# Kernel tuning notes

Hardware: AMD Instinct MI355X
Metric: run time of the kernel (lower is better)

## Reference

```python
import jax, jax.numpy as jnp
import numpy as np

B, N, D_IN, H, R = 4096, 32, 256, 256, 3
VIRTUAL_DECAY = 0.7


def setup_inputs() -> dict:
    key = jax.random.key(0)
    ks = jax.random.split(key, 16)
    def xavier(k, shape):
        fan_in, fan_out = shape[-1], shape[-2]
        lim = np.sqrt(6.0 / (fan_in + fan_out))
        return jax.random.uniform(k, shape, jnp.float32, -lim, lim)
    return {
        'input_vec': jax.random.normal(ks[0], (B, D_IN), jnp.float32),
        'child_h': jax.random.normal(ks[1], (B, N, H), jnp.float32),
        'child_c': jax.random.normal(ks[2], (B, N, H), jnp.float32),
        'relation_ids': jax.random.randint(ks[3], (B, N), 0, R, jnp.int32),
        'virtual_mask': jax.random.randint(ks[4], (B, N), 0, 2, jnp.int32).astype(bool),
        'rel_emb': xavier(ks[5], (R, H)),
        'W_i': xavier(ks[6], (H, D_IN + H)), 'b_i': jnp.full((H,), 0.1, jnp.float32),
        'W_f': xavier(ks[7], (R, H, H)),     'b_f': jnp.full((R, H), 0.1, jnp.float32),
        'W_o': xavier(ks[8], (H, D_IN + H)), 'b_o': jnp.full((H,), 0.1, jnp.float32),
        'W_u': xavier(ks[9], (H, D_IN + H)), 'b_u': jnp.full((H,), 0.1, jnp.float32),
        'w_att': xavier(ks[10], (1, H)).reshape(H), 'b_att': jnp.full((1,), 0.1, jnp.float32),
    }


def reference(input_vec, child_h, child_c, relation_ids, virtual_mask,
              rel_emb, W_i, b_i, W_f, b_f, W_o, b_o, W_u, b_u, w_att, b_att):
    # virtual-node decay applied to both child states
    decay = jnp.where(virtual_mask, VIRTUAL_DECAY, 1.0)[..., None]          # (B,N,1)
    ch = child_h * decay                                                     # (B,N,H)
    cc = child_c * decay                                                     # (B,N,H)

    # relation-aware attention over children (softmax over child axis)
    re = rel_emb[relation_ids]                                               # (B,N,H)
    scores = jnp.einsum('bnh,h->bn', re + ch, w_att) + b_att[0]              # (B,N)
    attn = jax.nn.softmax(scores, axis=1)[..., None]                         # (B,N,1)
    child_h_sum = jnp.sum(ch * attn, axis=1)                                 # (B,H)

    # relation-routed forget gates: compute all R linears, gather by relation id
    # NOTE: original applies NO sigmoid to f (faithful to source)
    f_all = jnp.einsum('bnh,rgh->bnrg', ch, W_f) + b_f                       # (B,N,R,H)
    f = jnp.take_along_axis(f_all, relation_ids[:, :, None, None], axis=2)[:, :, 0, :]  # (B,N,H)
    child_c_sum = jnp.sum(f * cc, axis=1)                                    # (B,H)

    combined = jnp.concatenate([input_vec, child_h_sum], axis=-1)            # (B,D_IN+H)
    i = jax.nn.sigmoid(combined @ W_i.T + b_i)
    o = jax.nn.sigmoid(combined @ W_o.T + b_o)
    u = jnp.tanh(combined @ W_u.T + b_u)
    c = i * u + child_c_sum
    h = o * jnp.tanh(c)
    return (h, c)
```

## Files before the change

kernel.cpp:

```cpp
#include <hip/hip_runtime.h>
#include <hip/hip_bf16.h>
#include <math.h>


#define B_    4096
#define N_    32
#define H_    256
#define DIN_  256
#define R_    3
#define MB    16
#define NBC   2
#define CHUNKS (MB / NBC)
#define DECAY 0.7f

#define WS_WF   0
#define WS_WI   196608
#define WS_WO   327680
#define WS_WU   458752
#define WS_ELEMS 589824

typedef __bf16 bf16;
typedef bf16  bf16x8 __attribute__((ext_vector_type(8)));
typedef float f32x4  __attribute__((ext_vector_type(4)));

__device__ __forceinline__ float sigmoidf_(float x) { return 1.0f / (1.0f + __expf(-x)); }

__device__ __forceinline__ bf16x8 cvt8_nt(const float* p) {
    f32x4 a = __builtin_nontemporal_load((const f32x4*)p);
    f32x4 b = __builtin_nontemporal_load((const f32x4*)(p + 4));
    bf16x8 r;
    #pragma unroll
    for (int j = 0; j < 4; ++j) { r[j] = (bf16)a[j]; r[j + 4] = (bf16)b[j]; }
    return r;
}
__device__ __forceinline__ bf16x8 cvt8_c(const float* p) {
    f32x4 a = *(const f32x4*)p;
    f32x4 b = *(const f32x4*)(p + 4);
    bf16x8 r;
    #pragma unroll
    for (int j = 0; j < 4; ++j) { r[j] = (bf16)a[j]; r[j + 4] = (bf16)b[j]; }
    return r;
}

template<bool WSW>
__device__ __forceinline__ bf16x8 ldw8(const bf16* wsp, const float* fp, int idx) {
    if constexpr (WSW) return *(const bf16x8*)(wsp + idx);
    else               return cvt8_c(fp + idx);
}

__global__ __launch_bounds__(256) void wprep(
    const float* __restrict__ Wf, const float* __restrict__ Wi,
    const float* __restrict__ Wo, const float* __restrict__ Wu,
    bf16* __restrict__ ws)
{
    int i = (blockIdx.x * 256 + threadIdx.x) * 8;
    const float* src; int off;
    if      (i < WS_WI) { src = Wf; off = i - WS_WF; }
    else if (i < WS_WO) { src = Wi; off = i - WS_WI; }
    else if (i < WS_WU) { src = Wo; off = i - WS_WO; }
    else                { src = Wu; off = i - WS_WU; }
    *(bf16x8*)(ws + i) = cvt8_c(src + off);
}

template<bool WSW>
__global__ __launch_bounds__(512, 4) void fused_main(
    const float* __restrict__ ivec,
    const float* __restrict__ child_h, const float* __restrict__ child_c,
    const int*  __restrict__ rel_ids,  const void* __restrict__ vmaskp,
    const float* __restrict__ rel_emb,
    const float* __restrict__ W_i, const float* __restrict__ b_i,
    const float* __restrict__ W_f, const float* __restrict__ b_f,
    const float* __restrict__ W_o, const float* __restrict__ b_o,
    const float* __restrict__ W_u, const float* __restrict__ b_u,
    const float* __restrict__ w_att, const float* __restrict__ b_att,
    const bf16* __restrict__ ws, float* __restrict__ out)
{
    __shared__ __align__(16) bf16 chs[NBC][N_][264];
    __shared__ __align__(16) bf16 hsumL[MB][264];
    __shared__ float csL[MB][H_];
    __shared__ float watt[H_];
    __shared__ float bfl[R_][H_];
    __shared__ float dall[MB][N_];
    __shared__ int   rids[MB][N_];
    __shared__ float scoreT[NBC][N_];
    __shared__ float attnd[NBC][N_];
    __shared__ float rdotL[4];
    __shared__ int   m8flag;

    const int tid  = threadIdx.x;
    const int wave = tid >> 6;
    const int lane = tid & 63;
    const int t    = lane & 15;
    const int q    = lane >> 4;
    const int b0   = blockIdx.x * MB;

    const bf16* wfb = ws + WS_WF;
    const bf16* wib = ws + WS_WI;
    const bf16* wob = ws + WS_WO;
    const bf16* wub = ws + WS_WU;

    if (tid < 64) {
        const unsigned char* vb = (const unsigned char*)vmaskp;
        int bad = vb[tid * 4 + 1] | vb[tid * 4 + 2] | vb[tid * 4 + 3];
        unsigned long long any = __ballot(bad != 0);
        if (tid == 0) m8flag = (any != 0ull) ? 1 : 0;
    }
    __syncthreads();

    if (tid < H_) watt[tid] = w_att[tid];
    {
        int idx = b0 * N_ + tid;
        rids[tid >> 5][tid & 31] = rel_ids[idx];
        bool vm = m8flag ? (((const unsigned char*)vmaskp)[idx] != 0)
                         : (((const int*)vmaskp)[idx] != 0);
        dall[tid >> 5][tid & 31] = vm ? DECAY : 1.0f;
    }
    if (tid >= 512 - R_ * 64 && false) {}
    for (int i = tid; i < R_ * H_; i += 512) ((float*)bfl)[i] = b_f[i];
    if (tid == 0) rdotL[3] = b_att[0];
    __syncthreads();

    if (wave < R_) {
        int r = wave;
        float p = 0.f;
        #pragma unroll
        for (int j = 0; j < 4; ++j) {
            int h = lane * 4 + j;
            p += rel_emb[r * H_ + h] * watt[h];
        }
        #pragma unroll
        for (int off = 32; off >= 1; off >>= 1) p += __shfl_xor(p, off);
        if (lane == 0) rdotL[r] = p;
    }

    for (int ck = 0; ck < CHUNKS; ++ck) {
        __syncthreads();

        {
            size_t base = (size_t)(b0 + ck * NBC) * (N_ * H_);
            #pragma unroll
            for (int it = 0; it < 4; ++it) {
                int ge = (it * 512 + tid) << 3;
                int bi = ge >> 13, n = (ge >> 8) & 31, h = ge & 255;
                *(bf16x8*)(&chs[bi][n][h]) = cvt8_nt(child_h + base + ge);
            }
        }
        __syncthreads();

        {
            int pair = tid >> 3, part = tid & 7;
            int bi = pair >> 5, n = pair & 31;
            const bf16* row = chs[bi][n];
            float p = 0.f;
            #pragma unroll
            for (int jj = 0; jj < 4; ++jj) {
                bf16x8 v = *(const bf16x8*)(&row[part * 32 + jj * 8]);
                #pragma unroll
                for (int j = 0; j < 8; ++j) p += (float)v[j] * watt[part * 32 + jj * 8 + j];
            }
            p += __shfl_xor(p, 1);
            p += __shfl_xor(p, 2);
            p += __shfl_xor(p, 4);
            if (part == 0) scoreT[bi][n] = p;
        }
        __syncthreads();

        if (tid < NBC * N_) {
            int bi = tid >> 5, n = tid & 31;
            int bl = ck * NBC + bi;
            float d = dall[bl][n];
            float s = d * scoreT[bi][n] + rdotL[rids[bl][n]] + rdotL[3];
            float m = s;
            #pragma unroll
            for (int off = 16; off >= 1; off >>= 1) m = fmaxf(m, __shfl_xor(m, off));
            float e = __expf(s - m);
            float sum = e;
            #pragma unroll
            for (int off = 16; off >= 1; off >>= 1) sum += __shfl_xor(sum, off);
            attnd[bi][n] = (e / sum) * d;
        }
        __syncthreads();

        {
            int bi = tid >> 8, g = tid & 255;
            int bl = ck * NBC + bi;
            float s = 0.f;
            #pragma unroll 8
            for (int n = 0; n < N_; ++n) s += attnd[bi][n] * (float)chs[bi][n][g];
            hsumL[bl][g] = (bf16)s;
        }

        f32x4 acc[2][4];
        #pragma unroll
        for (int i = 0; i < 2; ++i)
            #pragma unroll
            for (int j = 0; j < 4; ++j)
                #pragma unroll
                for (int c = 0; c < 4; ++c) acc[i][j][c] = 0.0f;

        bf16x8 bzero;
        #pragma unroll
        for (int i = 0; i < 8; ++i) bzero[i] = (bf16)0.0f;

        int myrid[4];
        #pragma unroll
        for (int nt = 0; nt < 4; ++nt)
            myrid[nt] = rids[ck * NBC + (nt >> 1)][((nt & 1) << 4) + t];

        #pragma unroll
        for (int kc = 0; kc < 8; ++kc) {
            const int k = kc * 32 + q * 8;
            bf16x8 v[4];
            #pragma unroll
            for (int nt = 0; nt < 4; ++nt)
                v[nt] = *(const bf16x8*)(&chs[nt >> 1][((nt & 1) << 4) + t][k]);
            #pragma unroll
            for (int r = 0; r < R_; ++r) {
                bf16x8 afrag[2];
                #pragma unroll
                for (int m2 = 0; m2 < 2; ++m2) {
                    int g = (wave * 2 + m2) * 16 + t;
                    afrag[m2] = ldw8<WSW>(wfb, W_f, (r * H_ + g) * H_ + k);
                }
                #pragma unroll
                for (int nt = 0; nt < 4; ++nt) {
                    bf16x8 vm = (myrid[nt] == r) ? v[nt] : bzero;
                    acc[0][nt] = __builtin_amdgcn_mfma_f32_16x16x32_bf16(afrag[0], vm, acc[0][nt], 0, 0, 0);
                    acc[1][nt] = __builtin_amdgcn_mfma_f32_16x16x32_bf16(afrag[1], vm, acc[1][nt], 0, 0, 0);
                }
            }
        }
        __syncthreads();

        {
            size_t base = (size_t)(b0 + ck * NBC) * (N_ * H_);
            #pragma unroll
            for (int it = 0; it < 4; ++it) {
                int ge = (it * 512 + tid) << 3;
                int bi = ge >> 13, n = (ge >> 8) & 31, h = ge & 255;
                *(bf16x8*)(&chs[bi][n][h]) = cvt8_nt(child_c + base + ge);
            }
        }
        __syncthreads();

        #pragma unroll
        for (int m2 = 0; m2 < 2; ++m2) {
            #pragma unroll
            for (int reg = 0; reg < 4; ++reg) {
                const int g = (wave * 2 + m2) * 16 + q * 4 + reg;
                #pragma unroll
                for (int bi = 0; bi < NBC; ++bi) {
                    int bl = ck * NBC + bi;
                    float p = 0.f;
                    #pragma unroll
                    for (int j = 0; j < 2; ++j) {
                        int nt = bi * 2 + j;
                        int n  = (j << 4) + t;
                        float Q   = acc[m2][nt][reg];
                        float d   = dall[bl][n];
                        float ccv = (float)chs[bi][n][g];
                        float bfv = bfl[rids[bl][n]][g];
                        p += ccv * d * fmaf(d, Q, bfv);
                    }
                    p += __shfl_xor(p, 1);
                    p += __shfl_xor(p, 2);
                    p += __shfl_xor(p, 4);
                    p += __shfl_xor(p, 8);
                    if (t == 0) csL[bl][g] = p;
                }
            }
        }
    }
    __syncthreads();

    const int j0 = wave * 32;
    f32x4 accI[2], accO[2], accU[2];
    #pragma unroll
    for (int c = 0; c < 2; ++c)
        #pragma unroll
        for (int r = 0; r < 4; ++r) { accI[c][r] = 0.f; accO[c][r] = 0.f; accU[c][r] = 0.f; }

    #pragma unroll
    for (int kc = 0; kc < 16; ++kc) {
        const int k = kc * 32 + q * 8;
        bf16x8 a;
        if (kc < 8) a = cvt8_nt(ivec + (size_t)(b0 + t) * DIN_ + k);
        else        a = *(const bf16x8*)(&hsumL[t][k - 256]);
        #pragma unroll
        for (int c = 0; c < 2; ++c) {
            int j = j0 + c * 16 + t;
            bf16x8 bI = ldw8<WSW>(wib, W_i, j * 512 + k);
            bf16x8 bO = ldw8<WSW>(wob, W_o, j * 512 + k);
            bf16x8 bU = ldw8<WSW>(wub, W_u, j * 512 + k);
            accI[c] = __builtin_amdgcn_mfma_f32_16x16x32_bf16(a, bI, accI[c], 0, 0, 0);
            accO[c] = __builtin_amdgcn_mfma_f32_16x16x32_bf16(a, bO, accO[c], 0, 0, 0);
            accU[c] = __builtin_amdgcn_mfma_f32_16x16x32_bf16(a, bU, accU[c], 0, 0, 0);
        }
    }

    #pragma unroll
    for (int c = 0; c < 2; ++c) {
        const int j = j0 + c * 16 + t;
        float biv = b_i[j], bov = b_o[j], buv = b_u[j];
        #pragma unroll
        for (int reg = 0; reg < 4; ++reg) {
            int bl = q * 4 + reg;
            size_t o1 = (size_t)(b0 + bl) * H_ + j;
            size_t o2 = (size_t)B_ * H_ + o1;
            float iv = sigmoidf_(accI[c][reg] + biv);
            float ov = sigmoidf_(accO[c][reg] + bov);
            float uv = tanhf(accU[c][reg] + buv);
            float cv = fmaf(iv, uv, csL[bl][j]);
            float hv = ov * tanhf(cv);
            __builtin_nontemporal_store(hv, out + o1);
            __builtin_nontemporal_store(cv, out + o2);
        }
    }
}

extern "C" void kernel_launch(void* const* d_in, const int* in_sizes, int n_in,
                              void* d_out, int out_size, void* d_ws, size_t ws_size,
                              hipStream_t stream)
{
    const float* ivec    = (const float*)d_in[0];
    const float* child_h = (const float*)d_in[1];
    const float* child_c = (const float*)d_in[2];
    const int*   relids  = (const int*)d_in[3];
    const void*  vmask   = d_in[4];
    const float* rel_emb = (const float*)d_in[5];
    const float* W_i     = (const float*)d_in[6];
    const float* b_i     = (const float*)d_in[7];
    const float* W_f     = (const float*)d_in[8];
    const float* b_f     = (const float*)d_in[9];
    const float* W_o     = (const float*)d_in[10];
    const float* b_o     = (const float*)d_in[11];
    const float* W_u     = (const float*)d_in[12];
    const float* b_u     = (const float*)d_in[13];
    const float* w_att   = (const float*)d_in[14];
    const float* b_att   = (const float*)d_in[15];
    float* out = (float*)d_out;
    bf16*  ws  = (bf16*)d_ws;

    const bool wsw = (ws_size >= (size_t)WS_ELEMS * sizeof(bf16));

    if (wsw) {
        hipLaunchKernelGGL(wprep, dim3(WS_ELEMS / 8 / 256), dim3(256), 0, stream,
                           W_f, W_i, W_o, W_u, ws);
        hipLaunchKernelGGL((fused_main<true>), dim3(B_ / MB), dim3(512), 0, stream,
                           ivec, child_h, child_c, relids, vmask, rel_emb,
                           W_i, b_i, W_f, b_f, W_o, b_o, W_u, b_u, w_att, b_att,
                           ws, out);
    } else {
        hipLaunchKernelGGL((fused_main<false>), dim3(B_ / MB), dim3(512), 0, stream,
                           ivec, child_h, child_c, relids, vmask, rel_emb,
                           W_i, b_i, W_f, b_f, W_o, b_o, W_u, b_u, w_att, b_att,
                           ws, out);
    }
}
```

Measured before the change: 484.7 us.

## Halve batch per block and prefetch child states into registers

Each block now handles 8 batch rows instead of 16, which doubles the grid and gives the GPU more blocks to keep it busy. The child_h and child_c loads are issued into registers early: child_c is fetched before the score and forget-gate MFMA work, and the next chunk's child_h is fetched during the reduction, so global memory latency overlaps with compute. The final gate GEMM still uses 16-row MFMA tiles, so half of its rows now duplicate real rows and only q<2 lanes store output. This wastes MFMA work and loads the weights once per 8 rows instead of per 16, which doubles total weight traffic. It also raises register pressure from the prefetch buffers.

```diff
diff --git a/kernel.cpp b/kernel.cpp
--- a/kernel.cpp
+++ b/kernel.cpp
@@ -8,7 +8,7 @@
 #define H_    256
 #define DIN_  256
 #define R_    3
-#define MB    16
+#define MB    8
 #define NBC   2
 #define CHUNKS (MB / NBC)
 #define DECAY 0.7f
@@ -107,15 +107,14 @@
     }
     __syncthreads();
 
-    if (tid < H_) watt[tid] = w_att[tid];
-    {
+    if (tid < 256) {
+        watt[tid] = w_att[tid];
         int idx = b0 * N_ + tid;
         rids[tid >> 5][tid & 31] = rel_ids[idx];
         bool vm = m8flag ? (((const unsigned char*)vmaskp)[idx] != 0)
                          : (((const int*)vmaskp)[idx] != 0);
         dall[tid >> 5][tid & 31] = vm ? DECAY : 1.0f;
     }
-    if (tid >= 512 - R_ * 64 && false) {}
     for (int i = tid; i < R_ * H_; i += 512) ((float*)bfl)[i] = b_f[i];
     if (tid == 0) rdotL[3] = b_att[0];
     __syncthreads();
@@ -133,19 +132,41 @@
         if (lane == 0) rdotL[r] = p;
     }
 
+    f32x4 hA[4], hB[4];
+    {
+        size_t base = (size_t)b0 * (N_ * H_);
+        #pragma unroll
+        for (int it = 0; it < 4; ++it) {
+            int ge = (it * 512 + tid) << 3;
+            hA[it] = __builtin_nontemporal_load((const f32x4*)(child_h + base + ge));
+            hB[it] = __builtin_nontemporal_load((const f32x4*)(child_h + base + ge + 4));
+        }
+    }
+
     for (int ck = 0; ck < CHUNKS; ++ck) {
         __syncthreads();
 
+        #pragma unroll
+        for (int it = 0; it < 4; ++it) {
+            int ge = (it * 512 + tid) << 3;
+            int bi = ge >> 13, n = (ge >> 8) & 31, h = ge & 255;
+            bf16x8 r;
+            #pragma unroll
+            for (int j = 0; j < 4; ++j) { r[j] = (bf16)hA[it][j]; r[j + 4] = (bf16)hB[it][j]; }
+            *(bf16x8*)(&chs[bi][n][h]) = r;
+        }
+        __syncthreads();
+
+        f32x4 cA[4], cB[4];
         {
             size_t base = (size_t)(b0 + ck * NBC) * (N_ * H_);
             #pragma unroll
             for (int it = 0; it < 4; ++it) {
                 int ge = (it * 512 + tid) << 3;
-                int bi = ge >> 13, n = (ge >> 8) & 31, h = ge & 255;
-                *(bf16x8*)(&chs[bi][n][h]) = cvt8_nt(child_h + base + ge);
-            }
-        }
-        __syncthreads();
+                cA[it] = __builtin_nontemporal_load((const f32x4*)(child_c + base + ge));
+                cB[it] = __builtin_nontemporal_load((const f32x4*)(child_c + base + ge + 4));
+            }
+        }
 
         {
             int pair = tid >> 3, part = tid & 7;
@@ -232,16 +253,26 @@
         }
         __syncthreads();
 
-        {
-            size_t base = (size_t)(b0 + ck * NBC) * (N_ * H_);
+        #pragma unroll
+        for (int it = 0; it < 4; ++it) {
+            int ge = (it * 512 + tid) << 3;
+            int bi = ge >> 13, n = (ge >> 8) & 31, h = ge & 255;
+            bf16x8 r;
+            #pragma unroll
+            for (int j = 0; j < 4; ++j) { r[j] = (bf16)cA[it][j]; r[j + 4] = (bf16)cB[it][j]; }
+            *(bf16x8*)(&chs[bi][n][h]) = r;
+        }
+        __syncthreads();
+
+        if (ck + 1 < CHUNKS) {
+            size_t base = (size_t)(b0 + (ck + 1) * NBC) * (N_ * H_);
             #pragma unroll
             for (int it = 0; it < 4; ++it) {
                 int ge = (it * 512 + tid) << 3;
-                int bi = ge >> 13, n = (ge >> 8) & 31, h = ge & 255;
-                *(bf16x8*)(&chs[bi][n][h]) = cvt8_nt(child_c + base + ge);
-            }
-        }
-        __syncthreads();
+                hA[it] = __builtin_nontemporal_load((const f32x4*)(child_h + base + ge));
+                hB[it] = __builtin_nontemporal_load((const f32x4*)(child_h + base + ge + 4));
+            }
+        }
 
         #pragma unroll
         for (int m2 = 0; m2 < 2; ++m2) {
@@ -274,6 +305,7 @@
     __syncthreads();
 
     const int j0 = wave * 32;
+    const int tt = t & 7;
     f32x4 accI[2], accO[2], accU[2];
     #pragma unroll
     for (int c = 0; c < 2; ++c)
@@ -284,8 +316,8 @@
     for (int kc = 0; kc < 16; ++kc) {
         const int k = kc * 32 + q * 8;
         bf16x8 a;
-        if (kc < 8) a = cvt8_nt(ivec + (size_t)(b0 + t) * DIN_ + k);
-        else        a = *(const bf16x8*)(&hsumL[t][k - 256]);
+        if (kc < 8) a = cvt8_nt(ivec + (size_t)(b0 + tt) * DIN_ + k);
+        else        a = *(const bf16x8*)(&hsumL[tt][k - 256]);
         #pragma unroll
         for (int c = 0; c < 2; ++c) {
             int j = j0 + c * 16 + t;
@@ -298,22 +330,24 @@
         }
     }
 
-    #pragma unroll
-    for (int c = 0; c < 2; ++c) {
-        const int j = j0 + c * 16 + t;
-        float biv = b_i[j], bov = b_o[j], buv = b_u[j];
-        #pragma unroll
-        for (int reg = 0; reg < 4; ++reg) {
-            int bl = q * 4 + reg;
-            size_t o1 = (size_t)(b0 + bl) * H_ + j;
-            size_t o2 = (size_t)B_ * H_ + o1;
-            float iv = sigmoidf_(accI[c][reg] + biv);
-            float ov = sigmoidf_(accO[c][reg] + bov);
-            float uv = tanhf(accU[c][reg] + buv);
-            float cv = fmaf(iv, uv, csL[bl][j]);
-            float hv = ov * tanhf(cv);
-            __builtin_nontemporal_store(hv, out + o1);
-            __builtin_nontemporal_store(cv, out + o2);
+    if (q < 2) {
+        #pragma unroll
+        for (int c = 0; c < 2; ++c) {
+            const int j = j0 + c * 16 + t;
+            float biv = b_i[j], bov = b_o[j], buv = b_u[j];
+            #pragma unroll
+            for (int reg = 0; reg < 4; ++reg) {
+                int bl = q * 4 + reg;
+                size_t o1 = (size_t)(b0 + bl) * H_ + j;
+                size_t o2 = (size_t)B_ * H_ + o1;
+                float iv = sigmoidf_(accI[c][reg] + biv);
+                float ov = sigmoidf_(accO[c][reg] + bov);
+                float uv = tanhf(accU[c][reg] + buv);
+                float cv = fmaf(iv, uv, csL[bl][j]);
+                float hv = ov * tanhf(cv);
+                __builtin_nontemporal_store(hv, out + o1);
+                __builtin_nontemporal_store(cv, out + o2);
+            }
         }
     }
 }
```

Result: slower. 547.0 us (+12.9%).
